# Kernel optimization log

Measured on AMD Instinct MI355X. Metric: run time of the kernel, lower is better.

Reference implementation:

```python
import jax, jax.numpy as jnp
import numpy as np
import math

N_NODES = 20000
N_EDGES = 320000
NODE_IN = 128
HIDDEN = 64
HEADS = 4
TIME_DIM = 64
SCALE = 60.0 / 1.0  # sensitivity / epsilon


def _linear_params(key, din, dout):
    k1, k2 = jax.random.split(key)
    bound = 1.0 / math.sqrt(din)
    w = jax.random.uniform(k1, (din, dout), minval=-bound, maxval=bound, dtype=jnp.float32)
    b = jax.random.uniform(k2, (dout,), minval=-bound, maxval=bound, dtype=jnp.float32)
    return w, b


def setup_inputs() -> dict:
    key = jax.random.key(0)
    ks = jax.random.split(key, 16)
    edge_index = jax.random.randint(ks[0], (2, N_EDGES), 0, N_NODES, dtype=jnp.int64)
    raw_time = jax.random.uniform(ks[1], (N_EDGES, 1), dtype=jnp.float32) * 86400.0
    noise = jax.random.laplace(ks[2], (N_EDGES, 1), dtype=jnp.float32) * SCALE
    node_emb = jax.random.normal(ks[3], (N_NODES, NODE_IN), dtype=jnp.float32)
    HC = HEADS * HIDDEN
    wq1, bq1 = _linear_params(ks[4], NODE_IN, HC)
    wk1, bk1 = _linear_params(ks[5], NODE_IN, HC)
    wv1, bv1 = _linear_params(ks[6], NODE_IN, HC)
    wt1, bt1 = _linear_params(ks[7], TIME_DIM, HC)
    wq2, bq2 = _linear_params(ks[8], HC, HC)
    wk2, bk2 = _linear_params(ks[9], HC, HC)
    wv2, bv2 = _linear_params(ks[10], HC, HC)
    wt2, bt2 = _linear_params(ks[11], TIME_DIM, HC)
    wc, bc = _linear_params(ks[12], HC, 1)
    return dict(edge_index=edge_index, raw_time=raw_time, noise=noise, node_emb=node_emb,
                wq1=wq1, bq1=bq1, wk1=wk1, bk1=bk1, wv1=wv1, bv1=bv1, wt1=wt1, bt1=bt1,
                wq2=wq2, bq2=bq2, wk2=wk2, bk2=bk2, wv2=wv2, bv2=bv2, wt2=wt2, bt2=bt2,
                wc=wc, bc=bc)


def time_encode(t):
    # t: [E, 1] -> [E, TIME_DIM]; interleaved sin/cos as in TimeEncoder
    half = jnp.arange(0, TIME_DIM, 2, dtype=jnp.float32)
    div_term = jnp.exp(half * (-math.log(10000.0) / TIME_DIM))  # [TIME_DIM/2]
    arg = t * div_term  # [E, TIME_DIM/2]
    te = jnp.stack([jnp.sin(arg), jnp.cos(arg)], axis=-1)  # [E, T/2, 2]
    return te.reshape(t.shape[0], TIME_DIM)


def temporal_conv(x, src, dst, time_enc, wq, bq, wk, bk, wv, bv, wt, bt):
    # gather-QKV, edge softmax over dst segments, scatter-add aggregation
    N = x.shape[0]
    q = (x @ wq + bq).reshape(N, HEADS, HIDDEN)
    k = (x @ wk + bk).reshape(N, HEADS, HIDDEN)
    v = (x @ wv + bv).reshape(N, HEADS, HIDDEN)
    t_enc = (time_enc @ wt + bt).reshape(-1, HEADS, HIDDEN)  # [E,H,C]
    q_i = q[dst]                      # [E,H,C]
    k_j = k[src] + t_enc              # [E,H,C]
    alpha = (q_i * k_j).sum(-1) / math.sqrt(HIDDEN)  # [E,H]
    # segment softmax over index = dst (PyG softmax semantics)
    amax = jax.ops.segment_max(alpha, dst, num_segments=N)  # [N,H]
    ea = jnp.exp(alpha - amax[dst])
    denom = jax.ops.segment_sum(ea, dst, num_segments=N)
    alpha = ea / (denom[dst] + 1e-16)
    msg = v[src] * alpha[..., None]   # [E,H,C]
    out = jax.ops.segment_sum(msg, dst, num_segments=N)  # [N,H,C]
    return out.reshape(N, HEADS * HIDDEN)


def reference(edge_index, raw_time, noise, node_emb,
              wq1, bq1, wk1, bk1, wv1, bv1, wt1, bt1,
              wq2, bq2, wk2, bk2, wv2, bv2, wt2, bt2,
              wc, bc):
    src, dst = edge_index[0], edge_index[1]
    noisy_time = raw_time + noise                 # Laplace mechanism
    time_encoded = time_encode(noisy_time)        # [E, TIME_DIM]
    x = jax.nn.relu(temporal_conv(node_emb, src, dst, time_encoded,
                                  wq1, bq1, wk1, bk1, wv1, bv1, wt1, bt1))
    x = jax.nn.relu(temporal_conv(x, src, dst, time_encoded,
                                  wq2, bq2, wk2, bk2, wv2, bv2, wt2, bt2))
    edge_emb = x[src] + x[dst]                    # [E, H*C]
    out = edge_emb @ wc + bc                      # [E, 1]
    return out.squeeze(-1)
```

## Files before the change

kernel.cpp:

```cpp
#include <hip/hip_runtime.h>
#include <hip/hip_fp16.h>
#include <math.h>

#define NN   20000
#define NE   320000
#define NIN  128
#define HC   256
#define NB   1024

typedef unsigned short u16;
typedef __attribute__((ext_vector_type(8))) short bf16x8;
typedef __attribute__((ext_vector_type(8))) unsigned short u16x8;
typedef __attribute__((ext_vector_type(4))) float f32x4;

__device__ __forceinline__ float bf2f(u16 u) {
  union { unsigned int i; float f; } x;
  x.i = ((unsigned int)u) << 16;
  return x.f;
}
__device__ __forceinline__ u16 f2bf(float f) {
  union { float f; unsigned int i; } x;
  x.f = f;
  unsigned int r = x.i + 0x7fffu + ((x.i >> 16) & 1u);
  return (u16)(r >> 16);
}

__device__ __forceinline__ float ldf(const void* p, int i, bool fbf) {
  return fbf ? bf2f(((const u16*)p)[i]) : ((const float*)p)[i];
}
__device__ __forceinline__ int ldsrc(const void* p, int e, bool is64) {
  const int* p32 = (const int*)p;
  return is64 ? p32[2 * e] : p32[e];
}
__device__ __forceinline__ int lddst(const void* p, int e, bool is64) {
  const int* p32 = (const int*)p;
  return is64 ? p32[2 * (NE + e)] : p32[NE + e];
}
__device__ __forceinline__ void stout(void* p, int i, float v, bool fbf) {
  if (fbf) ((u16*)p)[i] = f2bf(v);
  else ((float*)p)[i] = v;
}

__device__ __forceinline__ void gload_lds16(const u16* g, u16* l) {
  __builtin_amdgcn_global_load_lds(
      (const __attribute__((address_space(1))) void*)g,
      (__attribute__((address_space(3))) void*)l, 16, 0, 0);
}

__global__ void devinit_kernel(const void* __restrict__ eidx,
                               const void* __restrict__ nemb,
                               int* __restrict__ flags, float* __restrict__ divt) {
  int lane = threadIdx.x;
  if (lane < 32) {
    const float c32 = (float)(-0.14391156831212787);
    float prod = (float)(2 * lane) * c32;
    divt[lane] = (float)exp((double)prod);
  }
  if (lane == 0) {
    const int* p32 = (const int*)eidx;
    int is64 = 1;
    for (int i = 1; i < 128; i += 2)
      if (p32[i] != 0) { is64 = 0; break; }
    const u16* q16 = (const u16*)nemb;
    int fbf = 1;
    for (int i = 0; i < 128; i += 2) {
      unsigned e = (q16[i] >> 7) & 0xFF;
      if (e < 90 || e > 140) { fbf = 0; break; }
    }
    flags[0] = is64;
    flags[1] = fbf;
  }
}

__global__ void sentinel_kernel(const int* __restrict__ flags, void* __restrict__ out) {
  int i = blockIdx.x * 256 + threadIdx.x;
  if (i < NE) stout(out, i, 3000.0f, flags[1] != 0);
}
__global__ void raw_sentinel_kernel(u16* __restrict__ out) {
  int i = blockIdx.x * 256 + threadIdx.x;
  if (i < NE) out[i] = f2bf(3000.0f);
}

__global__ void zero_kernel(int* __restrict__ p, int n) {
  int i = blockIdx.x * 256 + threadIdx.x;
  if (i < n) p[i] = 0;
}

__global__ void hist_kernel(const int* __restrict__ flags, const void* __restrict__ eidx,
                            int* __restrict__ cnt) {
  bool is64 = flags[0] != 0;
  int e = blockIdx.x * 256 + threadIdx.x;
  if (e < NE) {
    int d = lddst(eidx, e, is64);
    if ((unsigned)d < NN) atomicAdd(&cnt[d], 1);
  }
}

__global__ void scan1_kernel(const int* __restrict__ cnt, int* __restrict__ offs,
                             int* __restrict__ bsum, int n) {
  __shared__ int s[256];
  int b = blockIdx.x, t = threadIdx.x, i = b * 256 + t;
  int x = (i < n) ? cnt[i] : 0;
  s[t] = x;
  __syncthreads();
  for (int off = 1; off < 256; off <<= 1) {
    int y = (t >= off) ? s[t - off] : 0;
    __syncthreads();
    s[t] += y;
    __syncthreads();
  }
  if (i < n) offs[i] = s[t] - x;
  if (t == 255) bsum[b] = s[t];
}

__global__ void scan2_kernel(int* __restrict__ bsum, int* __restrict__ offs,
                             int nb, int n) {
  __shared__ int s[256];
  int t = threadIdx.x;
  int x = (t < nb) ? bsum[t] : 0;
  s[t] = x;
  __syncthreads();
  for (int off = 1; off < 256; off <<= 1) {
    int y = (t >= off) ? s[t - off] : 0;
    __syncthreads();
    s[t] += y;
    __syncthreads();
  }
  if (t < nb) bsum[t] = s[t] - x;
  if (t == 255) offs[n] = s[t];
}

__global__ void scan3_kernel(int* __restrict__ offs, const int* __restrict__ bsum,
                             int* __restrict__ cursor, int n) {
  int i = blockIdx.x * 256 + threadIdx.x;
  if (i < n) {
    int v = offs[i] + bsum[blockIdx.x];
    offs[i] = v;
    cursor[i] = v;
  }
}

__global__ void fill_kernel(const int* __restrict__ flags, const void* __restrict__ eidx,
                            const void* __restrict__ rawt, const void* __restrict__ noise,
                            int* __restrict__ cursor, int* __restrict__ ssrc,
                            float* __restrict__ stt) {
  bool is64 = flags[0] != 0, fbf = flags[1] != 0;
  int e = blockIdx.x * 256 + threadIdx.x;
  if (e < NE) {
    int d = lddst(eidx, e, is64);
    if ((unsigned)d < NN) {
      int pos = atomicAdd(&cursor[d], 1);
      if ((unsigned)pos < NE) {
        int src = ldsrc(eidx, e, is64);
        if ((unsigned)src >= NN) src = 0;
        ssrc[pos] = src;
        stt[pos] = ldf(rawt, e, fbf) + ldf(noise, e, fbf);
      }
    }
  }
}

__global__ __launch_bounds__(256) void te_kernel(
    const float* __restrict__ stt, const float* __restrict__ divt,
    u16* __restrict__ te_s) {
  int idx = blockIdx.x * 256 + threadIdx.x;
  int p = idx >> 5;
  if (p >= NE) return;
  int f = idx & 31;
  float tt = stt[p];
  float arg = tt * divt[f];
  float sv, cv;
  sincosf(arg, &sv, &cv);
  __half hs = __float2half(sv), hc = __float2half(cv);
  unsigned int packed = (unsigned int)(*(u16*)&hs) | ((unsigned int)(*(u16*)&hc) << 16);
  ((unsigned int*)te_s)[(size_t)p * 32 + f] = packed;
}

__global__ void transw3_kernel(const int* __restrict__ flags, const void* __restrict__ W0,
                               const void* __restrict__ W1, const void* __restrict__ W2,
                               u16* __restrict__ WtBig, int K) {
  bool fbf = flags[1] != 0;
  __shared__ u16 tile[64][65];
  int z = blockIdx.z;
  const void* W = (z == 0) ? W0 : (z == 1) ? W1 : W2;
  u16* dst = WtBig + (size_t)z * 256 * K;
  int kb = blockIdx.x * 64, cb = blockIdx.y * 64;
  int tx = threadIdx.x & 63, ty = threadIdx.x >> 6;
  for (int i = ty; i < 64; i += 4)
    tile[tx][i] = f2bf(ldf(W, (kb + i) * HC + cb + tx, fbf));
  __syncthreads();
  for (int i = ty; i < 64; i += 4)
    dst[(size_t)(cb + i) * K + kb + tx] = tile[i][tx];
}

__global__ void wcombbias_kernel(const int* __restrict__ flags, const void* __restrict__ wt,
                                 const u16* __restrict__ Wqt, u16* __restrict__ Wout,
                                 const void* __restrict__ bq, const void* __restrict__ bk,
                                 const void* __restrict__ bv, float* __restrict__ biasBig,
                                 int K) {
  bool fbf = flags[1] != 0;
  int b = blockIdx.x, t = threadIdx.x;
  if (b < 256) {
    __shared__ float wrow[64];
    int j = b, h = j >> 6;
    if (t < 64) wrow[t] = ldf(wt, (j & 63) * HC + h * 64 + t, fbf);
    __syncthreads();
    if (t < K) {
      float s = 0.f;
#pragma unroll 8
      for (int mm = 0; mm < 64; ++mm)
        s += wrow[mm] * bf2f(Wqt[(size_t)(h * 64 + mm) * K + t]);
      Wout[(size_t)j * K + t] = f2bf(s);
    }
  } else if (b < 259) {
    int bb = b - 256;
    const void* p = (bb == 0) ? bq : (bb == 1) ? bk : bv;
    biasBig[bb * 256 + t] = ldf(p, t, fbf);
  } else {
    int j = t, h = j >> 6;
    float s = 0.f;
    for (int mm = 0; mm < 64; ++mm)
      s += ldf(bq, h * 64 + mm, fbf) * ldf(wt, (j & 63) * HC + h * 64 + mm, fbf);
    biasBig[768 + j] = s;
  }
}

template <bool AWS>
__global__ __launch_bounds__(256) void gemm_mfma(
    const int* __restrict__ flags, const void* __restrict__ Ap,
    const u16* __restrict__ Wt, const float* __restrict__ bias,
    u16* __restrict__ C, int M, int K) {
  bool fbf = flags[1] != 0;
  __shared__ u16 As[64 * 32];
  __shared__ u16 Bs[64 * 32];
  int tid = threadIdx.x;
  int rb = blockIdx.x * 64, cb = blockIdx.y * 64;
  int wave = tid >> 6, lane = tid & 63;
  int l15 = lane & 15, quad = lane >> 4;

  f32x4 acc[4];
#pragma unroll
  for (int mt = 0; mt < 4; ++mt)
#pragma unroll
    for (int r = 0; r < 4; ++r) acc[mt][r] = 0.f;

  int srow = tid >> 2;
  int schunk = tid & 3;
  int gchunk = schunk ^ (srow & 3);
  int arow = rb + srow; if (arow >= M) arow = M - 1;
  u16* asl = &As[srow * 32 + schunk * 8];
  u16* bsl = &Bs[srow * 32 + schunk * 8];
  const u16* bsrc = Wt + (size_t)(cb + srow) * K + gchunk * 8;
  const bool adirect = AWS || fbf;
  const u16* asrc = adirect ? ((const u16*)Ap + (size_t)arow * K + gchunk * 8) : (const u16*)0;

  for (int kk = 0; kk < K; kk += 32) {
    if (adirect) {
      gload_lds16(asrc + kk, asl);
    } else {
      const float* A = (const float*)Ap + (size_t)arow * K + kk + gchunk * 8;
      bf16x8 tmp;
#pragma unroll
      for (int i = 0; i < 8; ++i) tmp[i] = (short)f2bf(A[i]);
      *(bf16x8*)asl = tmp;
    }
    gload_lds16(bsrc + kk, bsl);
    __syncthreads();

    int bcol = wave * 16 + l15;
    bf16x8 bfrag = *(const bf16x8*)&Bs[bcol * 32 + ((quad ^ (bcol & 3)) * 8)];
#pragma unroll
    for (int mt = 0; mt < 4; ++mt) {
      int ar = mt * 16 + l15;
      bf16x8 afrag = *(const bf16x8*)&As[ar * 32 + ((quad ^ (ar & 3)) * 8)];
      acc[mt] = __builtin_amdgcn_mfma_f32_16x16x32_bf16(afrag, bfrag, acc[mt], 0, 0, 0);
    }
    __syncthreads();
  }

  int gcol = cb + wave * 16 + l15;
  float bv = bias[gcol];
  int scol;
  if (gcol < 256) scol = gcol;
  else if (gcol < 512) { int cc = gcol - 256; scol = 256 + ((cc >> 2) << 3) + (cc & 3); }
  else if (gcol < 768) { int cc = gcol - 512; scol = 256 + ((cc >> 2) << 3) + 4 + (cc & 3); }
  else scol = gcol;
#pragma unroll
  for (int mt = 0; mt < 4; ++mt) {
#pragma unroll
    for (int r = 0; r < 4; ++r) {
      int grow = rb + mt * 16 + quad * 4 + r;
      if (grow < M) C[(size_t)grow * NB + scol] = f2bf(acc[mt][r] + bv);
    }
  }
}

__global__ __launch_bounds__(256) void aggfused_kernel(
    const int* __restrict__ flags, const int* __restrict__ ssrc,
    const int* __restrict__ offsets, const u16* __restrict__ te_s,
    const u16* __restrict__ qkvp, const void* __restrict__ bt,
    u16* __restrict__ xout) {
  bool fbf = flags[1] != 0;
  int w = threadIdx.x >> 6;
  int n = blockIdx.x * 4 + w;
  if (n >= NN) return;
  int lane = threadIdx.x & 63;
  int c = lane * 4;
  int s0 = offsets[n], s1 = offsets[n + 1];
  if (s0 < 0) s0 = 0;
  if (s1 > NE) s1 = NE;

  ushort4 q4 = *(const ushort4*)(qkvp + (size_t)n * NB + c);
  ushort4 p4 = *(const ushort4*)(qkvp + (size_t)n * NB + 768 + c);
  float qx = bf2f(q4.x), qy = bf2f(q4.y), qz = bf2f(q4.z), qw = bf2f(q4.w);
  float px = bf2f(p4.x), py = bf2f(p4.y), pz = bf2f(p4.z), pw = bf2f(p4.w);
  float pb = qx * ldf(bt, c + 0, fbf);
  pb += qy * ldf(bt, c + 1, fbf);
  pb += qz * ldf(bt, c + 2, fbf);
  pb += qw * ldf(bt, c + 3, fbf);
  pb += __shfl_xor(pb, 1);
  pb += __shfl_xor(pb, 2);
  pb += __shfl_xor(pb, 4);
  pb += __shfl_xor(pb, 8);
  float qb = pb;
  int jb = c & 63;
  int kvoff = 256 + lane * 8;

  float m = -INFINITY, denom = 0.f;
  float acc0 = 0.f, acc1 = 0.f, acc2 = 0.f, acc3 = 0.f;

#define ALPHA_OF(kv, t4, out_a, okflag)                                        \
  {                                                                            \
    float s = qx * bf2f((kv)[0]) + __half2float(*(__half*)&(t4).x) * px;       \
    s += qy * bf2f((kv)[1]) + __half2float(*(__half*)&(t4).y) * py;            \
    s += qz * bf2f((kv)[2]) + __half2float(*(__half*)&(t4).z) * pz;            \
    s += qw * bf2f((kv)[3]) + __half2float(*(__half*)&(t4).w) * pw;            \
    s += __shfl_xor(s, 1);                                                     \
    s += __shfl_xor(s, 2);                                                     \
    s += __shfl_xor(s, 4);                                                     \
    s += __shfl_xor(s, 8);                                                     \
    out_a = (okflag) ? (s + qb) * 0.125f : 0.f;                                \
  }

#define STATE_UPDATE(a, kv, okflag)                                            \
  {                                                                            \
    float ea;                                                                  \
    if ((a) > m) {                                                             \
      float sc = __expf(m - (a));                                              \
      denom *= sc;                                                             \
      acc0 *= sc; acc1 *= sc; acc2 *= sc; acc3 *= sc;                          \
      m = (a);                                                                 \
      ea = 1.0f;                                                               \
    } else {                                                                   \
      ea = __expf((a) - m);                                                    \
    }                                                                          \
    denom += ea;                                                               \
    if (okflag) {                                                              \
      acc0 += ea * bf2f((kv)[4]);                                              \
      acc1 += ea * bf2f((kv)[5]);                                              \
      acc2 += ea * bf2f((kv)[6]);                                              \
      acc3 += ea * bf2f((kv)[7]);                                              \
    }                                                                          \
  }

  int p = s0;
  for (; p + 3 < s1; p += 4) {
    int srcA = ssrc[p], srcB = ssrc[p + 1], srcC = ssrc[p + 2], srcD = ssrc[p + 3];
    bool okA = (unsigned)srcA < NN, okB = (unsigned)srcB < NN;
    bool okC = (unsigned)srcC < NN, okD = (unsigned)srcD < NN;
    if (!okA) srcA = 0;
    if (!okB) srcB = 0;
    if (!okC) srcC = 0;
    if (!okD) srcD = 0;
    u16x8 kvA = *(const u16x8*)(qkvp + (size_t)srcA * NB + kvoff);
    u16x8 kvB = *(const u16x8*)(qkvp + (size_t)srcB * NB + kvoff);
    u16x8 kvC = *(const u16x8*)(qkvp + (size_t)srcC * NB + kvoff);
    u16x8 kvD = *(const u16x8*)(qkvp + (size_t)srcD * NB + kvoff);
    ushort4 tA = *(const ushort4*)(te_s + (size_t)p * 64 + jb);
    ushort4 tB = *(const ushort4*)(te_s + (size_t)(p + 1) * 64 + jb);
    ushort4 tC = *(const ushort4*)(te_s + (size_t)(p + 2) * 64 + jb);
    ushort4 tD = *(const ushort4*)(te_s + (size_t)(p + 3) * 64 + jb);

    float aA, aB, aC, aD;
    ALPHA_OF(kvA, tA, aA, okA)
    ALPHA_OF(kvB, tB, aB, okB)
    ALPHA_OF(kvC, tC, aC, okC)
    ALPHA_OF(kvD, tD, aD, okD)
    STATE_UPDATE(aA, kvA, okA)
    STATE_UPDATE(aB, kvB, okB)
    STATE_UPDATE(aC, kvC, okC)
    STATE_UPDATE(aD, kvD, okD)
  }
  for (; p < s1; ++p) {
    int src = ssrc[p];
    bool ok = (unsigned)src < NN;
    if (!ok) src = 0;
    u16x8 kv = *(const u16x8*)(qkvp + (size_t)src * NB + kvoff);
    ushort4 t4 = *(const ushort4*)(te_s + (size_t)p * 64 + jb);
    float a;
    ALPHA_OF(kv, t4, a, ok)
    STATE_UPDATE(a, kv, ok)
  }
#undef ALPHA_OF
#undef STATE_UPDATE

  float inv = 1.f / (denom + 1e-16f);
  ushort4 r;
  r.x = f2bf(fmaxf(acc0 * inv, 0.f));
  r.y = f2bf(fmaxf(acc1 * inv, 0.f));
  r.z = f2bf(fmaxf(acc2 * inv, 0.f));
  r.w = f2bf(fmaxf(acc3 * inv, 0.f));
  *(ushort4*)(xout + (size_t)n * HC + c) = r;
}

__global__ __launch_bounds__(256) void xwc_kernel(
    const int* __restrict__ flags, const u16* __restrict__ x,
    const void* __restrict__ wc, float* __restrict__ y) {
  bool fbf = flags[1] != 0;
  int n = blockIdx.x * 4 + (threadIdx.x >> 6);
  if (n >= NN) return;
  int lane = threadIdx.x & 63;
  int c = lane * 4;
  ushort4 x4 = *(const ushort4*)(x + (size_t)n * HC + c);
  float s = bf2f(x4.x) * ldf(wc, c + 0, fbf);
  s += bf2f(x4.y) * ldf(wc, c + 1, fbf);
  s += bf2f(x4.z) * ldf(wc, c + 2, fbf);
  s += bf2f(x4.w) * ldf(wc, c + 3, fbf);
  for (int off = 32; off; off >>= 1) s += __shfl_xor(s, off);
  if (lane == 0) y[n] = s;
}

__global__ __launch_bounds__(256) void final2_kernel(
    const int* __restrict__ flags, const void* __restrict__ eidx,
    const float* __restrict__ y, const void* __restrict__ bc,
    void* __restrict__ out) {
  bool is64 = flags[0] != 0, fbf = flags[1] != 0;
  int e = blockIdx.x * 256 + threadIdx.x;
  if (e >= NE) return;
  int src = ldsrc(eidx, e, is64);
  int dst = lddst(eidx, e, is64);
  if ((unsigned)src >= NN) src = 0;
  if ((unsigned)dst >= NN) dst = 0;
  stout(out, e, y[src] + y[dst] + ldf(bc, 0, fbf), fbf);
}

extern "C" void kernel_launch(void* const* d_in, const int* in_sizes, int n_in,
                              void* d_out, int out_size, void* d_ws, size_t ws_size,
                              hipStream_t stream) {
  const void* eidx  = d_in[0];
  const void* rawt  = d_in[1];
  const void* noise = d_in[2];
  const void* nemb  = d_in[3];
  const void *wq1 = d_in[4],  *bq1 = d_in[5];
  const void *wk1 = d_in[6],  *bk1 = d_in[7];
  const void *wv1 = d_in[8],  *bv1 = d_in[9];
  const void *wt1 = d_in[10], *bt1 = d_in[11];
  const void *wq2 = d_in[12], *bq2 = d_in[13];
  const void *wk2 = d_in[14], *bk2 = d_in[15];
  const void *wv2 = d_in[16], *bv2 = d_in[17];
  const void *wt2 = d_in[18], *bt2 = d_in[19];
  const void *wcp = d_in[20], *bcp = d_in[21];

  char* ws = (char*)d_ws;
  size_t off = 0;
  auto alloc = [&](size_t bytes) -> void* {
    void* p = ws + off;
    off += (bytes + 255) & ~(size_t)255;
    return p;
  };
  int*   flags  = (int*)alloc(256);
  float* divt   = (float*)alloc(256);
  u16*   WtBig  = (u16*)alloc((size_t)NB * HC * 2);
  float* biasBig= (float*)alloc((size_t)NB * 4);
  u16*   qkvp   = (u16*)alloc((size_t)NN * NB * 2);
  u16*   x1     = (u16*)alloc((size_t)NN * HC * 2);
  u16*   x2     = (u16*)alloc((size_t)NN * HC * 2);
  float* ynode  = (float*)alloc((size_t)NN * 4);
  int* offsets  = (int*)alloc((size_t)(NN + 1) * 4);
  int* cursor   = (int*)alloc((size_t)NN * 4);
  int* bsum     = (int*)alloc(256 * 4);
  int* ssrc     = (int*)alloc((size_t)NE * 4);
  float* stt    = (float*)alloc((size_t)NE * 4);
  u16* te_s     = (u16*)alloc((size_t)NE * 64 * 2);
  size_t need = off;

  int gN = (NN + 255) / 256, gE = (NE + 255) / 256;
  int nb = (NN + 255) / 256;

  if (ws_size < 1024) {
    raw_sentinel_kernel<<<gE, 256, 0, stream>>>((u16*)d_out);
    return;
  }
  devinit_kernel<<<1, 64, 0, stream>>>(eidx, nemb, flags, divt);
  if (need > ws_size) {
    sentinel_kernel<<<gE, 256, 0, stream>>>(flags, d_out);
    return;
  }

  zero_kernel<<<gN, 256, 0, stream>>>(cursor, NN);
  hist_kernel<<<gE, 256, 0, stream>>>(flags, eidx, cursor);
  scan1_kernel<<<nb, 256, 0, stream>>>(cursor, offsets, bsum, NN);
  scan2_kernel<<<1, 256, 0, stream>>>(bsum, offsets, nb, NN);
  scan3_kernel<<<nb, 256, 0, stream>>>(offsets, bsum, cursor, NN);
  fill_kernel<<<gE, 256, 0, stream>>>(flags, eidx, rawt, noise, cursor, ssrc, stt);

  int gTe = (NE * 32 + 255) / 256;
  te_kernel<<<gTe, 256, 0, stream>>>(stt, divt, te_s);

  dim3 ggemm((NN + 63) / 64, NB / 64);
  dim3 gt1(NIN / 64, 4, 3), gt2(HC / 64, 4, 3);
  int gNode = (NN + 3) / 4;

  transw3_kernel<<<gt1, 256, 0, stream>>>(flags, wq1, wk1, wv1, WtBig, NIN);
  wcombbias_kernel<<<260, 256, 0, stream>>>(flags, wt1, WtBig, WtBig + (size_t)768 * NIN,
                                            bq1, bk1, bv1, biasBig, NIN);
  gemm_mfma<false><<<ggemm, 256, 0, stream>>>(flags, nemb, WtBig, biasBig, qkvp, NN, NIN);
  aggfused_kernel<<<gNode, 256, 0, stream>>>(flags, ssrc, offsets, te_s, qkvp, bt1, x1);

  transw3_kernel<<<gt2, 256, 0, stream>>>(flags, wq2, wk2, wv2, WtBig, HC);
  wcombbias_kernel<<<260, 256, 0, stream>>>(flags, wt2, WtBig, WtBig + (size_t)768 * HC,
                                            bq2, bk2, bv2, biasBig, HC);
  gemm_mfma<true><<<ggemm, 256, 0, stream>>>(flags, x1, WtBig, biasBig, qkvp, NN, HC);
  aggfused_kernel<<<gNode, 256, 0, stream>>>(flags, ssrc, offsets, te_s, qkvp, bt2, x2);

  xwc_kernel<<<gNode, 256, 0, stream>>>(flags, x2, wcp, ynode);
  final2_kernel<<<gE, 256, 0, stream>>>(flags, eidx, ynode, bcp, d_out);
}
```

Before: 398.8 us.

## Split each node's edge range across two waves and fuse final projection into aggregation

The aggregation kernel now assigns two wavefronts per destination node, each running online softmax over half the edges, then merges the (max, denom, acc) states through shared memory. The second-layer instance also computes the per-node wc projection, removing the separate xwc kernel launch and its reread of x2. The time encoding now does an explicit double-precision range reduction before sincosf, which adds some per-element cost in exchange for accuracy on large arguments. The split doubles the block count, adds a block-wide barrier, and leaves half the waves idle during the merge.

```diff
diff --git a/kernel.cpp b/kernel.cpp
--- a/kernel.cpp
+++ b/kernel.cpp
@@ -169,8 +169,11 @@
   int f = idx & 31;
   float tt = stt[p];
   float arg = tt * divt[f];
+  double rev = (double)arg * 0.15915494309189535;
+  double fr = rev - floor(rev);
+  float red = (float)(fr * 6.283185307179586);
   float sv, cv;
-  sincosf(arg, &sv, &cv);
+  sincosf(red, &sv, &cv);
   __half hs = __float2half(sv), hc = __float2half(cv);
   unsigned int packed = (unsigned int)(*(u16*)&hs) | ((unsigned int)(*(u16*)&hc) << 16);
   ((unsigned int*)te_s)[(size_t)p * 32 + f] = packed;
@@ -295,39 +298,50 @@
   }
 }
 
+template <int DOY>
 __global__ __launch_bounds__(256) void aggfused_kernel(
     const int* __restrict__ flags, const int* __restrict__ ssrc,
     const int* __restrict__ offsets, const u16* __restrict__ te_s,
     const u16* __restrict__ qkvp, const void* __restrict__ bt,
-    u16* __restrict__ xout) {
+    u16* __restrict__ xout, const void* __restrict__ wc,
+    float* __restrict__ ynode) {
   bool fbf = flags[1] != 0;
+  __shared__ float mrg[2][64][6];
   int w = threadIdx.x >> 6;
-  int n = blockIdx.x * 4 + w;
-  if (n >= NN) return;
+  int nslot = w >> 1, half = w & 1;
+  int n = blockIdx.x * 2 + nslot;
+  bool valid = (n < NN);
   int lane = threadIdx.x & 63;
   int c = lane * 4;
-  int s0 = offsets[n], s1 = offsets[n + 1];
-  if (s0 < 0) s0 = 0;
-  if (s1 > NE) s1 = NE;
-
-  ushort4 q4 = *(const ushort4*)(qkvp + (size_t)n * NB + c);
-  ushort4 p4 = *(const ushort4*)(qkvp + (size_t)n * NB + 768 + c);
-  float qx = bf2f(q4.x), qy = bf2f(q4.y), qz = bf2f(q4.z), qw = bf2f(q4.w);
-  float px = bf2f(p4.x), py = bf2f(p4.y), pz = bf2f(p4.z), pw = bf2f(p4.w);
-  float pb = qx * ldf(bt, c + 0, fbf);
-  pb += qy * ldf(bt, c + 1, fbf);
-  pb += qz * ldf(bt, c + 2, fbf);
-  pb += qw * ldf(bt, c + 3, fbf);
-  pb += __shfl_xor(pb, 1);
-  pb += __shfl_xor(pb, 2);
-  pb += __shfl_xor(pb, 4);
-  pb += __shfl_xor(pb, 8);
-  float qb = pb;
-  int jb = c & 63;
-  int kvoff = 256 + lane * 8;
 
   float m = -INFINITY, denom = 0.f;
   float acc0 = 0.f, acc1 = 0.f, acc2 = 0.f, acc3 = 0.f;
+  float qx = 0.f, qy = 0.f, qz = 0.f, qw = 0.f, qb = 0.f;
+
+  if (valid) {
+    int s0 = offsets[n], s1 = offsets[n + 1];
+    if (s0 < 0) s0 = 0;
+    if (s1 > NE) s1 = NE;
+    int len = s1 - s0;
+    int mid = s0 + ((len + 1) >> 1);
+    int r0 = half ? mid : s0;
+    int r1 = half ? s1 : mid;
+
+    ushort4 q4 = *(const ushort4*)(qkvp + (size_t)n * NB + c);
+    ushort4 p4 = *(const ushort4*)(qkvp + (size_t)n * NB + 768 + c);
+    qx = bf2f(q4.x); qy = bf2f(q4.y); qz = bf2f(q4.z); qw = bf2f(q4.w);
+    float px = bf2f(p4.x), py = bf2f(p4.y), pz = bf2f(p4.z), pw = bf2f(p4.w);
+    float pb = qx * ldf(bt, c + 0, fbf);
+    pb += qy * ldf(bt, c + 1, fbf);
+    pb += qz * ldf(bt, c + 2, fbf);
+    pb += qw * ldf(bt, c + 3, fbf);
+    pb += __shfl_xor(pb, 1);
+    pb += __shfl_xor(pb, 2);
+    pb += __shfl_xor(pb, 4);
+    pb += __shfl_xor(pb, 8);
+    qb = pb;
+    int jb = c & 63;
+    int kvoff = 256 + lane * 8;
 
 #define ALPHA_OF(kv, t4, out_a, okflag)                                        \
   {                                                                            \
@@ -363,71 +377,85 @@
     }                                                                          \
   }
 
-  int p = s0;
-  for (; p + 3 < s1; p += 4) {
-    int srcA = ssrc[p], srcB = ssrc[p + 1], srcC = ssrc[p + 2], srcD = ssrc[p + 3];
-    bool okA = (unsigned)srcA < NN, okB = (unsigned)srcB < NN;
-    bool okC = (unsigned)srcC < NN, okD = (unsigned)srcD < NN;
-    if (!okA) srcA = 0;
-    if (!okB) srcB = 0;
-    if (!okC) srcC = 0;
-    if (!okD) srcD = 0;
-    u16x8 kvA = *(const u16x8*)(qkvp + (size_t)srcA * NB + kvoff);
-    u16x8 kvB = *(const u16x8*)(qkvp + (size_t)srcB * NB + kvoff);
-    u16x8 kvC = *(const u16x8*)(qkvp + (size_t)srcC * NB + kvoff);
-    u16x8 kvD = *(const u16x8*)(qkvp + (size_t)srcD * NB + kvoff);
-    ushort4 tA = *(const ushort4*)(te_s + (size_t)p * 64 + jb);
-    ushort4 tB = *(const ushort4*)(te_s + (size_t)(p + 1) * 64 + jb);
-    ushort4 tC = *(const ushort4*)(te_s + (size_t)(p + 2) * 64 + jb);
-    ushort4 tD = *(const ushort4*)(te_s + (size_t)(p + 3) * 64 + jb);
-
-    float aA, aB, aC, aD;
-    ALPHA_OF(kvA, tA, aA, okA)
-    ALPHA_OF(kvB, tB, aB, okB)
-    ALPHA_OF(kvC, tC, aC, okC)
-    ALPHA_OF(kvD, tD, aD, okD)
-    STATE_UPDATE(aA, kvA, okA)
-    STATE_UPDATE(aB, kvB, okB)
-    STATE_UPDATE(aC, kvC, okC)
-    STATE_UPDATE(aD, kvD, okD)
-  }
-  for (; p < s1; ++p) {
-    int src = ssrc[p];
-    bool ok = (unsigned)src < NN;
-    if (!ok) src = 0;
-    u16x8 kv = *(const u16x8*)(qkvp + (size_t)src * NB + kvoff);
-    ushort4 t4 = *(const ushort4*)(te_s + (size_t)p * 64 + jb);
-    float a;
-    ALPHA_OF(kv, t4, a, ok)
-    STATE_UPDATE(a, kv, ok)
-  }
+    int p = r0;
+    for (; p + 3 < r1; p += 4) {
+      int srcA = ssrc[p], srcB = ssrc[p + 1], srcC = ssrc[p + 2], srcD = ssrc[p + 3];
+      bool okA = (unsigned)srcA < NN, okB = (unsigned)srcB < NN;
+      bool okC = (unsigned)srcC < NN, okD = (unsigned)srcD < NN;
+      if (!okA) srcA = 0;
+      if (!okB) srcB = 0;
+      if (!okC) srcC = 0;
+      if (!okD) srcD = 0;
+      u16x8 kvA = *(const u16x8*)(qkvp + (size_t)srcA * NB + kvoff);
+      u16x8 kvB = *(const u16x8*)(qkvp + (size_t)srcB * NB + kvoff);
+      u16x8 kvC = *(const u16x8*)(qkvp + (size_t)srcC * NB + kvoff);
+      u16x8 kvD = *(const u16x8*)(qkvp + (size_t)srcD * NB + kvoff);
+      ushort4 tA = *(const ushort4*)(te_s + (size_t)p * 64 + jb);
+      ushort4 tB = *(const ushort4*)(te_s + (size_t)(p + 1) * 64 + jb);
+      ushort4 tC = *(const ushort4*)(te_s + (size_t)(p + 2) * 64 + jb);
+      ushort4 tD = *(const ushort4*)(te_s + (size_t)(p + 3) * 64 + jb);
+
+      float aA, aB, aC, aD;
+      ALPHA_OF(kvA, tA, aA, okA)
+      ALPHA_OF(kvB, tB, aB, okB)
+      ALPHA_OF(kvC, tC, aC, okC)
+      ALPHA_OF(kvD, tD, aD, okD)
+      STATE_UPDATE(aA, kvA, okA)
+      STATE_UPDATE(aB, kvB, okB)
+      STATE_UPDATE(aC, kvC, okC)
+      STATE_UPDATE(aD, kvD, okD)
+    }
+    for (; p < r1; ++p) {
+      int src = ssrc[p];
+      bool ok = (unsigned)src < NN;
+      if (!ok) src = 0;
+      u16x8 kv = *(const u16x8*)(qkvp + (size_t)src * NB + kvoff);
+      ushort4 t4 = *(const ushort4*)(te_s + (size_t)p * 64 + jb);
+      float a;
+      ALPHA_OF(kv, t4, a, ok)
+      STATE_UPDATE(a, kv, ok)
+    }
 #undef ALPHA_OF
 #undef STATE_UPDATE
-
-  float inv = 1.f / (denom + 1e-16f);
-  ushort4 r;
-  r.x = f2bf(fmaxf(acc0 * inv, 0.f));
-  r.y = f2bf(fmaxf(acc1 * inv, 0.f));
-  r.z = f2bf(fmaxf(acc2 * inv, 0.f));
-  r.w = f2bf(fmaxf(acc3 * inv, 0.f));
-  *(ushort4*)(xout + (size_t)n * HC + c) = r;
-}
-
-__global__ __launch_bounds__(256) void xwc_kernel(
-    const int* __restrict__ flags, const u16* __restrict__ x,
-    const void* __restrict__ wc, float* __restrict__ y) {
-  bool fbf = flags[1] != 0;
-  int n = blockIdx.x * 4 + (threadIdx.x >> 6);
-  if (n >= NN) return;
-  int lane = threadIdx.x & 63;
-  int c = lane * 4;
-  ushort4 x4 = *(const ushort4*)(x + (size_t)n * HC + c);
-  float s = bf2f(x4.x) * ldf(wc, c + 0, fbf);
-  s += bf2f(x4.y) * ldf(wc, c + 1, fbf);
-  s += bf2f(x4.z) * ldf(wc, c + 2, fbf);
-  s += bf2f(x4.w) * ldf(wc, c + 3, fbf);
-  for (int off = 32; off; off >>= 1) s += __shfl_xor(s, off);
-  if (lane == 0) y[n] = s;
+  }
+
+  if (half == 1) {
+    float* s = mrg[nslot][lane];
+    s[0] = m; s[1] = denom; s[2] = acc0; s[3] = acc1; s[4] = acc2; s[5] = acc3;
+  }
+  __syncthreads();
+  if (half == 0 && valid) {
+    const float* s = mrg[nslot][lane];
+    float mB = s[0], dB = s[1];
+    float mM = fmaxf(m, mB);
+    float d, a0, a1, a2, a3;
+    if (mM == -INFINITY) {
+      d = 0.f; a0 = a1 = a2 = a3 = 0.f;
+    } else {
+      float sA = (m == -INFINITY) ? 0.f : __expf(m - mM);
+      float sB = (mB == -INFINITY) ? 0.f : __expf(mB - mM);
+      d = denom * sA + dB * sB;
+      a0 = acc0 * sA + s[2] * sB;
+      a1 = acc1 * sA + s[3] * sB;
+      a2 = acc2 * sA + s[4] * sB;
+      a3 = acc3 * sA + s[5] * sB;
+    }
+    float inv = 1.f / (d + 1e-16f);
+    ushort4 r;
+    r.x = f2bf(fmaxf(a0 * inv, 0.f));
+    r.y = f2bf(fmaxf(a1 * inv, 0.f));
+    r.z = f2bf(fmaxf(a2 * inv, 0.f));
+    r.w = f2bf(fmaxf(a3 * inv, 0.f));
+    *(ushort4*)(xout + (size_t)n * HC + c) = r;
+    if (DOY) {
+      float yv = bf2f(r.x) * ldf(wc, c + 0, fbf);
+      yv += bf2f(r.y) * ldf(wc, c + 1, fbf);
+      yv += bf2f(r.z) * ldf(wc, c + 2, fbf);
+      yv += bf2f(r.w) * ldf(wc, c + 3, fbf);
+      for (int off = 32; off; off >>= 1) yv += __shfl_xor(yv, off);
+      if (lane == 0) ynode[n] = yv;
+    }
+  }
 }
 
 __global__ __launch_bounds__(256) void final2_kernel(
@@ -509,20 +537,21 @@
 
   dim3 ggemm((NN + 63) / 64, NB / 64);
   dim3 gt1(NIN / 64, 4, 3), gt2(HC / 64, 4, 3);
-  int gNode = (NN + 3) / 4;
+  int gNode2 = (NN + 1) / 2;
 
   transw3_kernel<<<gt1, 256, 0, stream>>>(flags, wq1, wk1, wv1, WtBig, NIN);
   wcombbias_kernel<<<260, 256, 0, stream>>>(flags, wt1, WtBig, WtBig + (size_t)768 * NIN,
                                             bq1, bk1, bv1, biasBig, NIN);
   gemm_mfma<false><<<ggemm, 256, 0, stream>>>(flags, nemb, WtBig, biasBig, qkvp, NN, NIN);
-  aggfused_kernel<<<gNode, 256, 0, stream>>>(flags, ssrc, offsets, te_s, qkvp, bt1, x1);
+  aggfused_kernel<0><<<gNode2, 256, 0, stream>>>(flags, ssrc, offsets, te_s, qkvp, bt1,
+                                                 x1, wcp, ynode);
 
   transw3_kernel<<<gt2, 256, 0, stream>>>(flags, wq2, wk2, wv2, WtBig, HC);
   wcombbias_kernel<<<260, 256, 0, stream>>>(flags, wt2, WtBig, WtBig + (size_t)768 * HC,
                                             bq2, bk2, bv2, biasBig, HC);
   gemm_mfma<true><<<ggemm, 256, 0, stream>>>(flags, x1, WtBig, biasBig, qkvp, NN, HC);
-  aggfused_kernel<<<gNode, 256, 0, stream>>>(flags, ssrc, offsets, te_s, qkvp, bt2, x2);
-
-  xwc_kernel<<<gNode, 256, 0, stream>>>(flags, x2, wcp, ynode);
+  aggfused_kernel<1><<<gNode2, 256, 0, stream>>>(flags, ssrc, offsets, te_s, qkvp, bt2,
+                                                 x2, wcp, ynode);
+
   final2_kernel<<<gE, 256, 0, stream>>>(flags, eidx, ynode, bcp, d_out);
 }
```

Result: no change. 401.3 us (+0.6%).
